# Kernel optimization log

Measured on AMD Instinct MI355X. Metric: run time of the kernel, lower is better.

The kernel has to match this reference:

```python
import jax, jax.numpy as jnp
import numpy as np

ALPHA_REC = 2.0
ALPHA_SMOOTH = 3.0


def setup_inputs() -> dict:
    key = jax.random.key(0)
    k1, k2 = jax.random.split(key)
    B, C, T, J = 2048, 3, 300, 25
    inputs = jax.random.normal(k1, (B, C, T, J), dtype=jnp.float32)
    targets = jax.random.normal(k2, (B, C, T, J), dtype=jnp.float32)
    return {"inputs": inputs, "targets": targets}


def _smooth_loss(inputs, targets):
    # torch permute(0,3,2,1): [B, C, T, J] -> [B, J, T, C]
    x = jnp.transpose(inputs, (0, 3, 2, 1))
    t = jnp.transpose(targets, (0, 3, 2, 1))
    J, T = x.shape[1], x.shape[2]
    # Faithful to source quirk: x[:, i, j] - x[:, i, j+1] ** 2 (next frame squared,
    # NOT squared difference), summed over j = 0..T-2.  Shapes: [B, J, C].
    sx = jnp.sum(x[:, :, :-1] - jnp.square(x[:, :, 1:]), axis=2)
    st = jnp.sum(t[:, :, :-1] - jnp.square(t[:, :, 1:]), axis=2)
    # Loop over i = 0..J-2 only (last joint excluded in the source).
    total = jnp.sum(jnp.abs(sx - st)[:, : J - 1], axis=1)  # [B, C]
    loss = jnp.sqrt(total) / (J * T)
    return jnp.mean(loss)


def reference(inputs, targets):
    loss_rec = jnp.mean(jnp.square(inputs - targets))
    loss_smooth = _smooth_loss(inputs, targets)
    return ALPHA_REC * loss_rec + ALPHA_SMOOTH * loss_smooth
```

## Files before the change

kernel.cpp:

```cpp
#include <hip/hip_runtime.h>
#include <math.h>

constexpr int B_ = 2048, C_ = 3, T_ = 300, J_ = 25;
constexpr int SLAB = T_ * J_;
constexpr int NBC  = B_ * C_;

__global__ __launch_bounds__(256) void fused_kernel(
    const float* __restrict__ gin, const float* __restrict__ gtg,
    float* __restrict__ rec_part, float* __restrict__ sm_part) {
  __shared__ float s_col[J_];
  __shared__ float s_red[4];

  const int tid  = threadIdx.x;
  const int lane = tid & 63;
  const int wave = tid >> 6;

  if (tid < J_) s_col[tid] = 0.f;
  __syncthreads();

  const size_t base = (size_t)blockIdx.x * SLAB;
  const float* in = gin + base;
  const float* tg = gtg + base;

  float rec = 0.f;
  float p0 = 0.f, p1 = 0.f, p2 = 0.f, p3 = 0.f;
  const int e0 = tid * 4;

  if (tid < 250) {
    #pragma unroll
    for (int it = 0; it < 8; ++it) {
      const int e = it * 1000 + e0;
      if (e < SLAB) {
        const float4 x = *(const float4*)(in + e);
        const float4 y = *(const float4*)(tg + e);
        { float d = x.x - y.x, s = x.x + y.x; rec += d * d;
          p0 += (e     < 7475 ? d : 0.f) - (e     >= 25 ? d * s : 0.f); }
        { float d = x.y - y.y, s = x.y + y.y; rec += d * d;
          p1 += (e + 1 < 7475 ? d : 0.f) - (e + 1 >= 25 ? d * s : 0.f); }
        { float d = x.z - y.z, s = x.z + y.z; rec += d * d;
          p2 += (e + 2 < 7475 ? d : 0.f) - (e + 2 >= 25 ? d * s : 0.f); }
        { float d = x.w - y.w, s = x.w + y.w; rec += d * d;
          p3 += (e + 3 < 7475 ? d : 0.f) - (e + 3 >= 25 ? d * s : 0.f); }
      }
    }
    const int j0 = (tid * 4) % 25;
    atomicAdd(&s_col[j0],            p0);
    atomicAdd(&s_col[(j0 + 1) % 25], p1);
    atomicAdd(&s_col[(j0 + 2) % 25], p2);
    atomicAdd(&s_col[(j0 + 3) % 25], p3);
  }

  #pragma unroll
  for (int off = 32; off > 0; off >>= 1) rec += __shfl_down(rec, off, 64);
  if (lane == 0) s_red[wave] = rec;
  __syncthreads();

  if (wave == 0) {
    float aval = (lane < J_ - 1) ? fabsf(s_col[lane]) : 0.f;
    #pragma unroll
    for (int off = 32; off > 0; off >>= 1) aval += __shfl_down(aval, off, 64);
    if (lane == 0) {
      rec_part[blockIdx.x] = s_red[0] + s_red[1] + s_red[2] + s_red[3];
      sm_part[blockIdx.x]  = sqrtf(aval);
    }
  }
}

__global__ __launch_bounds__(256) void finalize_kernel(
    const float* __restrict__ rec_part, const float* __restrict__ sm_part,
    float* __restrict__ out) {
  const int tid  = threadIdx.x;
  const int lane = tid & 63;
  const int wave = tid >> 6;
  double r = 0.0, s = 0.0;
  for (int i = tid; i < NBC; i += 256) {
    r += (double)rec_part[i];
    s += (double)sm_part[i];
  }
  #pragma unroll
  for (int off = 32; off > 0; off >>= 1) {
    r += __shfl_down(r, off, 64);
    s += __shfl_down(s, off, 64);
  }
  __shared__ double sr[4], ss[4];
  if (lane == 0) { sr[wave] = r; ss[wave] = s; }
  __syncthreads();
  if (tid == 0) {
    const double rt = sr[0] + sr[1] + sr[2] + sr[3];
    const double st = ss[0] + ss[1] + ss[2] + ss[3];
    const double loss_rec    = rt / (double)((long long)B_ * C_ * T_ * J_);
    const double loss_smooth = (st / (double)NBC) / (double)(J_ * T_);
    out[0] = (float)(2.0 * loss_rec + 3.0 * loss_smooth);
  }
}

extern "C" void kernel_launch(void* const* d_in, const int* in_sizes, int n_in,
                              void* d_out, int out_size, void* d_ws, size_t ws_size,
                              hipStream_t stream) {
  const float* in = (const float*)d_in[0];
  const float* tg = (const float*)d_in[1];
  float* rec_part = (float*)d_ws;
  float* sm_part  = rec_part + NBC;
  fused_kernel<<<NBC, 256, 0, stream>>>(in, tg, rec_part, sm_part);
  finalize_kernel<<<1, 256, 0, stream>>>(rec_part, sm_part, (float*)d_out);
}
```

Baseline: 369.5 us.

## Process eight (b,c) slabs per block with peeled boundary iterations

Each block now handles 8 consecutive (b,c) slabs instead of one, so there are 768 blocks rather than 6144, with per-slab shared accumulators and per-wave final reductions. The first and last row iterations are peeled so the interior loop uses a branch-free d*(1-s) update, and the last partial row is guarded by tid<125 instead of a per-iteration bounds check. This cuts launch/tail overhead and per-element predication, at the cost of fewer blocks (768 on 256 CUs) and a longer serial loop per block, which may reduce latency hiding for this memory-bound reduction.

```diff
diff --git a/kernel.cpp b/kernel.cpp
--- a/kernel.cpp
+++ b/kernel.cpp
@@ -4,50 +4,75 @@
 constexpr int B_ = 2048, C_ = 3, T_ = 300, J_ = 25;
 constexpr int SLAB = T_ * J_;
 constexpr int NBC  = B_ * C_;
+constexpr int G    = 8;
+constexpr int NBLK = NBC / G;
 
-__global__ __launch_bounds__(256) void fused_kernel(
+__global__ __launch_bounds__(256, 3) void fused_kernel(
     const float* __restrict__ gin, const float* __restrict__ gtg,
     float* __restrict__ rec_part, float* __restrict__ sm_part) {
-  __shared__ float s_col[J_];
+  __shared__ float s_col[G * J_];
   __shared__ float s_red[4];
 
   const int tid  = threadIdx.x;
   const int lane = tid & 63;
   const int wave = tid >> 6;
 
-  if (tid < J_) s_col[tid] = 0.f;
+  for (int i = tid; i < G * J_; i += 256) s_col[i] = 0.f;
   __syncthreads();
 
-  const size_t base = (size_t)blockIdx.x * SLAB;
-  const float* in = gin + base;
-  const float* tg = gtg + base;
-
+  const int slab0 = blockIdx.x * G;
+  const int e0    = tid * 4;
   float rec = 0.f;
-  float p0 = 0.f, p1 = 0.f, p2 = 0.f, p3 = 0.f;
-  const int e0 = tid * 4;
 
   if (tid < 250) {
+    const int b0 = e0 % 25, b1 = (e0 + 1) % 25, b2 = (e0 + 2) % 25, b3 = (e0 + 3) % 25;
+    const bool q0 = (e0    ) >= 25, q1 = (e0 + 1) >= 25,
+               q2 = (e0 + 2) >= 25, q3 = (e0 + 3) >= 25;
+    const bool l0 = (e0    ) < 475, l1 = (e0 + 1) < 475,
+               l2 = (e0 + 2) < 475, l3 = (e0 + 3) < 475;
+
     #pragma unroll
-    for (int it = 0; it < 8; ++it) {
-      const int e = it * 1000 + e0;
-      if (e < SLAB) {
+    for (int g = 0; g < G; ++g) {
+      const size_t base = (size_t)(slab0 + g) * SLAB;
+      const float* in = gin + base;
+      const float* tg = gtg + base;
+      float c0 = 0.f, c1 = 0.f, c2 = 0.f, c3 = 0.f;
+
+      {
+        const float4 x = *(const float4*)(in + e0);
+        const float4 y = *(const float4*)(tg + e0);
+        float d, s;
+        d = x.x - y.x; s = x.x + y.x; rec += d * d; c0 += d - (q0 ? d * s : 0.f);
+        d = x.y - y.y; s = x.y + y.y; rec += d * d; c1 += d - (q1 ? d * s : 0.f);
+        d = x.z - y.z; s = x.z + y.z; rec += d * d; c2 += d - (q2 ? d * s : 0.f);
+        d = x.w - y.w; s = x.w + y.w; rec += d * d; c3 += d - (q3 ? d * s : 0.f);
+      }
+      #pragma unroll
+      for (int it = 1; it < 7; ++it) {
+        const int e = it * 1000 + e0;
         const float4 x = *(const float4*)(in + e);
         const float4 y = *(const float4*)(tg + e);
-        { float d = x.x - y.x, s = x.x + y.x; rec += d * d;
-          p0 += (e     < 7475 ? d : 0.f) - (e     >= 25 ? d * s : 0.f); }
-        { float d = x.y - y.y, s = x.y + y.y; rec += d * d;
-          p1 += (e + 1 < 7475 ? d : 0.f) - (e + 1 >= 25 ? d * s : 0.f); }
-        { float d = x.z - y.z, s = x.z + y.z; rec += d * d;
-          p2 += (e + 2 < 7475 ? d : 0.f) - (e + 2 >= 25 ? d * s : 0.f); }
-        { float d = x.w - y.w, s = x.w + y.w; rec += d * d;
-          p3 += (e + 3 < 7475 ? d : 0.f) - (e + 3 >= 25 ? d * s : 0.f); }
+        float d, s;
+        d = x.x - y.x; s = x.x + y.x; rec += d * d; c0 += d * (1.f - s);
+        d = x.y - y.y; s = x.y + y.y; rec += d * d; c1 += d * (1.f - s);
+        d = x.z - y.z; s = x.z + y.z; rec += d * d; c2 += d * (1.f - s);
+        d = x.w - y.w; s = x.w + y.w; rec += d * d; c3 += d * (1.f - s);
       }
+      if (tid < 125) {
+        const int e = 7000 + e0;
+        const float4 x = *(const float4*)(in + e);
+        const float4 y = *(const float4*)(tg + e);
+        float d, s;
+        d = x.x - y.x; s = x.x + y.x; rec += d * d; c0 += (l0 ? d : 0.f) - d * s;
+        d = x.y - y.y; s = x.y + y.y; rec += d * d; c1 += (l1 ? d : 0.f) - d * s;
+        d = x.z - y.z; s = x.z + y.z; rec += d * d; c2 += (l2 ? d : 0.f) - d * s;
+        d = x.w - y.w; s = x.w + y.w; rec += d * d; c3 += (l3 ? d : 0.f) - d * s;
+      }
+      atomicAdd(&s_col[g * 25 + b0], c0);
+      atomicAdd(&s_col[g * 25 + b1], c1);
+      atomicAdd(&s_col[g * 25 + b2], c2);
+      atomicAdd(&s_col[g * 25 + b3], c3);
     }
-    const int j0 = (tid * 4) % 25;
-    atomicAdd(&s_col[j0],            p0);
-    atomicAdd(&s_col[(j0 + 1) % 25], p1);
-    atomicAdd(&s_col[(j0 + 2) % 25], p2);
-    atomicAdd(&s_col[(j0 + 3) % 25], p3);
   }
 
   #pragma unroll
@@ -55,15 +80,15 @@
   if (lane == 0) s_red[wave] = rec;
   __syncthreads();
 
-  if (wave == 0) {
-    float aval = (lane < J_ - 1) ? fabsf(s_col[lane]) : 0.f;
+  #pragma unroll
+  for (int g = wave; g < G; g += 4) {
+    float v = (lane < J_ - 1) ? fabsf(s_col[g * 25 + lane]) : 0.f;
     #pragma unroll
-    for (int off = 32; off > 0; off >>= 1) aval += __shfl_down(aval, off, 64);
-    if (lane == 0) {
-      rec_part[blockIdx.x] = s_red[0] + s_red[1] + s_red[2] + s_red[3];
-      sm_part[blockIdx.x]  = sqrtf(aval);
-    }
+    for (int off = 32; off > 0; off >>= 1) v += __shfl_down(v, off, 64);
+    if (lane == 0) sm_part[slab0 + g] = sqrtf(v);
   }
+  if (tid == 0)
+    rec_part[blockIdx.x] = s_red[0] + s_red[1] + s_red[2] + s_red[3];
 }
 
 __global__ __launch_bounds__(256) void finalize_kernel(
@@ -73,10 +98,8 @@
   const int lane = tid & 63;
   const int wave = tid >> 6;
   double r = 0.0, s = 0.0;
-  for (int i = tid; i < NBC; i += 256) {
-    r += (double)rec_part[i];
-    s += (double)sm_part[i];
-  }
+  for (int i = tid; i < NBLK; i += 256) r += (double)rec_part[i];
+  for (int i = tid; i < NBC;  i += 256) s += (double)sm_part[i];
   #pragma unroll
   for (int off = 32; off > 0; off >>= 1) {
     r += __shfl_down(r, off, 64);
@@ -100,7 +123,7 @@
   const float* in = (const float*)d_in[0];
   const float* tg = (const float*)d_in[1];
   float* rec_part = (float*)d_ws;
-  float* sm_part  = rec_part + NBC;
-  fused_kernel<<<NBC, 256, 0, stream>>>(in, tg, rec_part, sm_part);
+  float* sm_part  = rec_part + NBLK;
+  fused_kernel<<<NBLK, 256, 0, stream>>>(in, tg, rec_part, sm_part);
   finalize_kernel<<<1, 256, 0, stream>>>(rec_part, sm_part, (float*)d_out);
 }
```

After: 376.4 us. No clear change (+1.9%).
